# Kernel optimization log

Measured on AMD Instinct MI355X. Metric: run time of the kernel, lower is better.

The kernel has to match this reference:

```python
import jax, jax.numpy as jnp
import numpy as np

EPS = 1e-12  # matches torch F.normalize default eps

def setup_inputs() -> dict:
    key = jax.random.key(0)
    k1, k2 = jax.random.split(key)
    n, d = 131072, 512
    x = jax.random.normal(k1, (n, d), dtype=jnp.float32)
    p = jax.random.normal(k2, (n, d), dtype=jnp.float32)
    scale = jnp.float32(5.0)
    return {"x": x, "p": p, "scale": scale}

def reference(x, p, scale):
    # F.normalize: v / max(||v||_2, eps), rowwise
    xn = x / jnp.maximum(jnp.linalg.norm(x, axis=-1, keepdims=True), EPS)
    pn = p / jnp.maximum(jnp.linalg.norm(p, axis=-1, keepdims=True), EPS)
    # diagonal of (xn @ pn.T) == rowwise dot product; compute directly in O(n*d)
    sim = jnp.einsum('nd,nd->n', xn, pn)
    return sim * scale
```

## Files before the change

kernel.cpp:

```cpp
#include <hip/hip_runtime.h>


#define EPSF 1e-12f

__global__ __launch_bounds__(256) void cossim_rows_kernel(
    const float* __restrict__ x,
    const float* __restrict__ p,
    const float* __restrict__ scale,
    float* __restrict__ out,
    int n)
{
    const int gwave = (int)((blockIdx.x * (unsigned)blockDim.x + threadIdx.x) >> 6);
    const int lane  = threadIdx.x & 63;
    if (gwave >= n) return;

    const float4* __restrict__ xr =
        reinterpret_cast<const float4*>(x + (size_t)gwave * 512);
    const float4* __restrict__ pr =
        reinterpret_cast<const float4*>(p + (size_t)gwave * 512);

    float xx = 0.f, pp = 0.f, xp = 0.f;

#pragma unroll
    for (int i = 0; i < 2; ++i) {
        float4 a = xr[lane + 64 * i];
        float4 b = pr[lane + 64 * i];
        xx += a.x * a.x + a.y * a.y + a.z * a.z + a.w * a.w;
        pp += b.x * b.x + b.y * b.y + b.z * b.z + b.w * b.w;
        xp += a.x * b.x + a.y * b.y + a.z * b.z + a.w * b.w;
    }

#pragma unroll
    for (int off = 32; off > 0; off >>= 1) {
        xx += __shfl_xor(xx, off, 64);
        pp += __shfl_xor(pp, off, 64);
        xp += __shfl_xor(xp, off, 64);
    }

    if (lane == 0) {
        float denom = fmaxf(sqrtf(xx), EPSF) * fmaxf(sqrtf(pp), EPSF);
        out[gwave] = xp / denom * scale[0];
    }
}

extern "C" void kernel_launch(void* const* d_in, const int* in_sizes, int n_in,
                              void* d_out, int out_size, void* d_ws, size_t ws_size,
                              hipStream_t stream) {
    const float* x     = (const float*)d_in[0];
    const float* p     = (const float*)d_in[1];
    const float* scale = (const float*)d_in[2];
    float* out = (float*)d_out;

    const int n = out_size;
    const int blocks = (n + 3) / 4;
    cossim_rows_kernel<<<blocks, 256, 0, stream>>>(x, p, scale, out, n);
}
```

Measured before the change: 94.40 us.

## Use persistent grid-stride waves with two rows per iteration and nontemporal loads

Replaces the one-row-per-wave launch with a fixed grid of 2048 blocks whose waves stride over rows, handling two rows per iteration so eight 16-byte loads are in flight before any reduction. Loads use nontemporal hints to avoid polluting the cache with streamed data, and the scale is read once per thread. The aim is more memory-level parallelism and less launch and tail overhead on a purely bandwidth-bound kernel. In exchange it uses more registers per thread and fixes a grid size that may not match the device's occupancy.

```diff
diff --git a/kernel.cpp b/kernel.cpp
--- a/kernel.cpp
+++ b/kernel.cpp
@@ -1,57 +1,103 @@
 #include <hip/hip_runtime.h>
 
 
+typedef float f32x4 __attribute__((ext_vector_type(4)));
+
 #define EPSF 1e-12f
 
+__device__ __forceinline__ f32x4 ntload(const f32x4* p) {
+    return __builtin_nontemporal_load(p);
+}
+
+__device__ __forceinline__ float dot4(f32x4 a, f32x4 b) {
+    return a.x * b.x + a.y * b.y + a.z * b.z + a.w * b.w;
+}
+
 __global__ __launch_bounds__(256) void cossim_rows_kernel(
-    const float* __restrict__ x,
-    const float* __restrict__ p,
+    const f32x4* __restrict__ x4,
+    const f32x4* __restrict__ p4,
     const float* __restrict__ scale,
     float* __restrict__ out,
-    int n)
+    int n, int nwaves)
 {
-    const int gwave = (int)((blockIdx.x * (unsigned)blockDim.x + threadIdx.x) >> 6);
-    const int lane  = threadIdx.x & 63;
-    if (gwave >= n) return;
+    const int wid  = (int)((blockIdx.x * 256u + threadIdx.x) >> 6);
+    const int lane = threadIdx.x & 63;
+    const float s  = scale[0];
 
-    const float4* __restrict__ xr =
-        reinterpret_cast<const float4*>(x + (size_t)gwave * 512);
-    const float4* __restrict__ pr =
-        reinterpret_cast<const float4*>(p + (size_t)gwave * 512);
+    int row = wid;
+    for (; row + nwaves < n; row += 2 * nwaves) {
+        const int row1 = row + nwaves;
+        const f32x4* xr0 = x4 + (size_t)row  * 128;
+        const f32x4* pr0 = p4 + (size_t)row  * 128;
+        const f32x4* xr1 = x4 + (size_t)row1 * 128;
+        const f32x4* pr1 = p4 + (size_t)row1 * 128;
 
-    float xx = 0.f, pp = 0.f, xp = 0.f;
+        f32x4 a0 = ntload(xr0 + lane);
+        f32x4 a1 = ntload(xr0 + lane + 64);
+        f32x4 b0 = ntload(pr0 + lane);
+        f32x4 b1 = ntload(pr0 + lane + 64);
+        f32x4 c0 = ntload(xr1 + lane);
+        f32x4 c1 = ntload(xr1 + lane + 64);
+        f32x4 d0 = ntload(pr1 + lane);
+        f32x4 d1 = ntload(pr1 + lane + 64);
+
+        float xx0 = dot4(a0, a0) + dot4(a1, a1);
+        float pp0 = dot4(b0, b0) + dot4(b1, b1);
+        float xp0 = dot4(a0, b0) + dot4(a1, b1);
+        float xx1 = dot4(c0, c0) + dot4(c1, c1);
+        float pp1 = dot4(d0, d0) + dot4(d1, d1);
+        float xp1 = dot4(c0, d0) + dot4(c1, d1);
 
 #pragma unroll
-    for (int i = 0; i < 2; ++i) {
-        float4 a = xr[lane + 64 * i];
-        float4 b = pr[lane + 64 * i];
-        xx += a.x * a.x + a.y * a.y + a.z * a.z + a.w * a.w;
-        pp += b.x * b.x + b.y * b.y + b.z * b.z + b.w * b.w;
-        xp += a.x * b.x + a.y * b.y + a.z * b.z + a.w * b.w;
+        for (int off = 32; off > 0; off >>= 1) {
+            xx0 += __shfl_xor(xx0, off, 64);
+            pp0 += __shfl_xor(pp0, off, 64);
+            xp0 += __shfl_xor(xp0, off, 64);
+            xx1 += __shfl_xor(xx1, off, 64);
+            pp1 += __shfl_xor(pp1, off, 64);
+            xp1 += __shfl_xor(xp1, off, 64);
+        }
+
+        if (lane == 0) {
+            out[row]  = xp0 / (fmaxf(sqrtf(xx0), EPSF) * fmaxf(sqrtf(pp0), EPSF)) * s;
+            out[row1] = xp1 / (fmaxf(sqrtf(xx1), EPSF) * fmaxf(sqrtf(pp1), EPSF)) * s;
+        }
     }
+    for (; row < n; row += nwaves) {
+        const f32x4* xr = x4 + (size_t)row * 128;
+        const f32x4* pr = p4 + (size_t)row * 128;
+
+        f32x4 a0 = ntload(xr + lane);
+        f32x4 a1 = ntload(xr + lane + 64);
+        f32x4 b0 = ntload(pr + lane);
+        f32x4 b1 = ntload(pr + lane + 64);
+
+        float xx = dot4(a0, a0) + dot4(a1, a1);
+        float pp = dot4(b0, b0) + dot4(b1, b1);
+        float xp = dot4(a0, b0) + dot4(a1, b1);
 
 #pragma unroll
-    for (int off = 32; off > 0; off >>= 1) {
-        xx += __shfl_xor(xx, off, 64);
-        pp += __shfl_xor(pp, off, 64);
-        xp += __shfl_xor(xp, off, 64);
-    }
+        for (int off = 32; off > 0; off >>= 1) {
+            xx += __shfl_xor(xx, off, 64);
+            pp += __shfl_xor(pp, off, 64);
+            xp += __shfl_xor(xp, off, 64);
+        }
 
-    if (lane == 0) {
-        float denom = fmaxf(sqrtf(xx), EPSF) * fmaxf(sqrtf(pp), EPSF);
-        out[gwave] = xp / denom * scale[0];
+        if (lane == 0)
+            out[row] = xp / (fmaxf(sqrtf(xx), EPSF) * fmaxf(sqrtf(pp), EPSF)) * s;
     }
 }
 
 extern "C" void kernel_launch(void* const* d_in, const int* in_sizes, int n_in,
                               void* d_out, int out_size, void* d_ws, size_t ws_size,
                               hipStream_t stream) {
-    const float* x     = (const float*)d_in[0];
-    const float* p     = (const float*)d_in[1];
+    const f32x4* x4    = (const f32x4*)d_in[0];
+    const f32x4* p4    = (const f32x4*)d_in[1];
     const float* scale = (const float*)d_in[2];
     float* out = (float*)d_out;
 
     const int n = out_size;
-    const int blocks = (n + 3) / 4;
-    cossim_rows_kernel<<<blocks, 256, 0, stream>>>(x, p, scale, out, n);
+    const int blocks = 2048;
+    const int nwaves = blocks * (256 / 64);
+    cossim_rows_kernel<<<blocks, 256, 0, stream>>>(x4, p4, scale, out, n, nwaves);
 }
```

After: 90.25 us. 4.4% less time.
